# Performance work log

Hardware: AMD Instinct MI355X
Metric: run time of the kernel (lower is better)

The kernel has to match this reference:

```python
import jax, jax.numpy as jnp
import numpy as np

N = 8          # num_nodes (forced: stack with deconv output of leading dim 64 = 8*8)
T = 10         # out_dim == num_steps (Conv1d(out_dim, 1, ...) runs over the time axis)
H = 64         # hidden_dim (forced: ConvTranspose1d in_channels=64)
E = 2 * N      # edges come in fwd/rev pairs; E/2 must equal N for avg_pool squeeze
NODE_IN = 512  # gat1 in_dim = x_feat width (510) + CNN_1 output (2)
EDGE_IN = 128


def _conv1d(x, w, b, pad):
    # x: [B, Cin, L], w: [Cout, Cin, K]
    y = jax.lax.conv_general_dilated(x, w, (1,), [(pad, pad)],
                                     dimension_numbers=('NCH', 'OIH', 'NCH'))
    return y + b[None, :, None]


def _gat(x, src, dst, ea, W, a_s, a_d, We, a_e, bias, heads, ch, concat):
    # PyG GATConv with edge_dim and default add_self_loops=True (mean-fill edge_attr)
    n = x.shape[0]
    loop = jnp.arange(n)
    src = jnp.concatenate([src, loop])
    dst = jnp.concatenate([dst, loop])
    ea = jnp.concatenate([ea, jnp.broadcast_to(ea.mean(0), (n, ea.shape[1]))], 0)
    h = (x @ W).reshape(n, heads, ch)                 # [N,H,C]
    he = (ea @ We).reshape(-1, heads, ch)             # [E+N,H,C]
    alpha = (h * a_s).sum(-1)[src] + (h * a_d).sum(-1)[dst] + (he * a_e).sum(-1)
    alpha = jax.nn.leaky_relu(alpha, 0.2)             # [E+N,H]
    amax = jax.ops.segment_max(alpha, dst, num_segments=n)
    ex = jnp.exp(alpha - amax[dst])
    den = jax.ops.segment_sum(ex, dst, num_segments=n)
    w = ex / (den[dst] + 1e-16)                       # scatter-softmax over dst
    out = jax.ops.segment_sum(w[:, :, None] * h[src], dst, num_segments=n)
    out = out.reshape(n, heads * ch) if concat else out.mean(1)
    return out + bias


def _forward(x_feat, x_feat_tmp, edge_attr, c1w1, c1b1, c1w2, c1b2,
             g1_lin, g1_as, g1_ad, g1_le, g1_ae, g1_b,
             g2_lin, g2_as, g2_ad, g2_le, g2_ae, g2_b,
             mlp_w1, mlp_b1, mlp_w2, mlp_b2,
             d1w, d1b, d2w, d2b, d3w, d3b,
             c2w1, c2b1, c2w2, c2b2, c2l1w, c2l1b, c2l2w, c2l2b,
             edge_index):
    src, dst = edge_index[0], edge_index[1]
    # ---- CNN_1 on rows 1 and 5 of x_feat_tmp ----
    t = jnp.stack([x_feat_tmp[1], x_feat_tmp[5]], axis=1)    # [N,2,T]
    t = t.reshape(2, N, T)                                   # torch .view semantics
    t = jax.nn.relu(_conv1d(t, c1w1, c1b1, 1))               # [2,N,T]
    t = _conv1d(jnp.transpose(t, (0, 2, 1)), c1w2, c1b2, 1)  # [2,1,N]
    x_ = jax.nn.relu(t.reshape(N, 2))                        # torch .view semantics
    # ---- GAT stack ----
    x = jnp.concatenate([x_feat, x_], axis=1)                # [N,512]
    x = jax.nn.relu(_gat(x, src, dst, edge_attr, g1_lin, g1_as, g1_ad,
                         g1_le, g1_ae, g1_b, 4, H, True))    # [N,256]
    ea_new = jax.nn.relu(edge_attr @ mlp_w1 + mlp_b1) @ mlp_w2 + mlp_b2  # [E,64]
    x = jax.nn.relu(_gat(x, src, dst, ea_new, g2_lin, g2_as, g2_ad,
                         g2_le, g2_ae, g2_b, 1, H, False))   # [N,64]
    # ---- ConvTranspose1d on length-1 input == einsum; avg_pool2d over nodes/edges ----
    x_pool = (jnp.einsum('ni,iot->not', x, d1w) + d1b[None, :, None]).mean(0)          # [64,10]
    ef = (jnp.einsum('ni,iot->not', ea_new[::2], d2w) + d2b[None, :, None]).mean(0)    # [64,10]
    er = (jnp.einsum('ni,iot->not', ea_new[1::2], d3w) + d3b[None, :, None]).mean(0)   # [64,10]
    inf = x_feat_tmp.reshape(N * N, T)                       # [64,10]
    # ---- CNN_2 ----
    c = jnp.stack([x_pool, inf, ef, er], axis=1)             # [64,4,10]
    c = _conv1d(c, c2w1, c2b1, 0)                            # [64,32,8]
    c = c.reshape(N * N, 32, 4, 2).max(-1)                   # MaxPool1d(2) -> [64,32,4]
    c = _conv1d(c, c2w2, c2b2, 0)                            # [64,64,2]
    c = c.reshape(N * N, 128)                                # Flatten(1,2)
    c = jax.nn.relu((c @ c2l1w + c2l1b) @ c2l2w + c2l2b)     # [64,10]
    return c.reshape(N, N, T)


def setup_inputs():
    ks = iter(jax.random.split(jax.random.key(0), 48))
    def rn(shape, s=0.1):
        return jax.random.normal(next(ks), shape, dtype=jnp.float32) * s
    return dict(
        x_feat=rn((N, NODE_IN - 2), 1.0),
        x_feat_tmp=rn((N, N, T), 1.0),
        edge_attr=rn((E, EDGE_IN), 1.0),
        c1w1=rn((N, N, 3)), c1b1=rn((N,)),
        c1w2=rn((1, T, 3)), c1b2=rn((1,)),
        g1_lin=rn((NODE_IN, 4 * H)), g1_as=rn((4, H)), g1_ad=rn((4, H)),
        g1_le=rn((EDGE_IN, 4 * H)), g1_ae=rn((4, H)), g1_b=rn((4 * H,)),
        g2_lin=rn((4 * H, H)), g2_as=rn((1, H)), g2_ad=rn((1, H)),
        g2_le=rn((H, H)), g2_ae=rn((1, H)), g2_b=rn((H,)),
        mlp_w1=rn((EDGE_IN, H)), mlp_b1=rn((H,)),
        mlp_w2=rn((H, H)), mlp_b2=rn((H,)),
        d1w=rn((H, H, 10)), d1b=rn((H,)),
        d2w=rn((H, H, 10)), d2b=rn((H,)),
        d3w=rn((H, H, 10)), d3b=rn((H,)),
        c2w1=rn((32, 4, 3)), c2b1=rn((32,)),
        c2w2=rn((64, 32, 3)), c2b2=rn((64,)),
        c2l1w=rn((128, 256)), c2l1b=rn((256,)),
        c2l2w=rn((256, T)), c2l2b=rn((T,)),
        edge_index=jax.random.randint(next(ks), (2, E), 0, N, dtype=jnp.int32),
    )


def reference(x_feat, x_feat_tmp, edge_attr, c1w1, c1b1, c1w2, c1b2,
              g1_lin, g1_as, g1_ad, g1_le, g1_ae, g1_b,
              g2_lin, g2_as, g2_ad, g2_le, g2_ae, g2_b,
              mlp_w1, mlp_b1, mlp_w2, mlp_b2,
              d1w, d1b, d2w, d2b, d3w, d3b,
              c2w1, c2b1, c2w2, c2b2, c2l1w, c2l1b, c2l2w, c2l2b,
              edge_index):
    return _forward(x_feat, x_feat_tmp, edge_attr, c1w1, c1b1, c1w2, c1b2,
                    g1_lin, g1_as, g1_ad, g1_le, g1_ae, g1_b,
                    g2_lin, g2_as, g2_ad, g2_le, g2_ae, g2_b,
                    mlp_w1, mlp_b1, mlp_w2, mlp_b2,
                    d1w, d1b, d2w, d2b, d3w, d3b,
                    c2w1, c2b1, c2w2, c2b2, c2l1w, c2l1b, c2l2w, c2l2b,
                    edge_index)
```

## Files before the change

kernel.cpp:

```cpp
#include <hip/hip_runtime.h>
#include <math.h>

#define WS_HXPART 0
#define WS_SMALL  8192
#define SM_XCNN 0
#define SM_SE1A 16
#define SM_SE1B 84
#define SM_SE2  152
#define SM_WF   172
#define SM_BF   1452
#define SM_VME  1462
#define SM_SIZE 1600

#define F_H    0
#define F_X1   2048
#define F_H2P  4096
#define F_GL0  6144
#define F_GL1  6400
#define F_G1AS 6656
#define F_G1AD 6912
#define F_G1B  7168
#define F_SS1  7424
#define F_SD1  7456
#define F_MX1  7488
#define F_DN1  7520
#define F_WT1  7552
#define F_SW2  7680
#define F_A1   7680
#define F_H2   7936
#define F_X2   8448
#define F_G2AS 8960
#define F_G2AD 9024
#define F_G2B  9088
#define F_SS2  9152
#define F_SD2  9160
#define F_MX2  9168
#define F_DN2  9176
#define F_A2   9184
#define F_WT2  9248
#define F_SML  13824
#define F_SW1  15424
#define F_CIN  15808
#define F_ESRC 15968
#define F_EDST 15992
#define F_SB1  16016
#define F_SB2  16048
#define F_SDB  16112
#define F_VM0  16128
#define SM_TOT 16192

__global__ __launch_bounds__(256) void k1_pre(
    const float* __restrict__ xf,   const float* __restrict__ xft,
    const float* __restrict__ ea,
    const float* __restrict__ c1w1, const float* __restrict__ c1b1,
    const float* __restrict__ c1w2, const float* __restrict__ c1b2,
    const float* __restrict__ g1lin,const float* __restrict__ g1le,
    const float* __restrict__ g1ae,
    const float* __restrict__ mw1,  const float* __restrict__ mb1,
    const float* __restrict__ mw2,  const float* __restrict__ mb2,
    const float* __restrict__ g2le, const float* __restrict__ g2ae,
    const float* __restrict__ l1w,  const float* __restrict__ l1b,
    const float* __restrict__ l2w,  const float* __restrict__ l2b,
    float* __restrict__ ws)
{
    const int b = blockIdx.x, tid = threadIdx.x;
    if (b < 4) {
        __shared__ float sx[1024];
        const int k0 = b * 128;
        const int klen = (b == 3) ? 126 : 128;
        for (int idx = tid; idx < 1024; idx += 256) {
            int n = idx >> 7, kk = idx & 127;
            sx[n * 128 + kk] = (kk < klen) ? xf[n * 510 + k0 + kk] : 0.f;
        }
        __syncthreads();
        float acc[8];
        #pragma unroll
        for (int n = 0; n < 8; ++n) acc[n] = 0.f;
        for (int kk = 0; kk < 128; ++kk) {
            float w = g1lin[(k0 + kk) * 256 + tid];
            #pragma unroll
            for (int n = 0; n < 8; ++n) acc[n] += sx[n * 128 + kk] * w;
        }
        #pragma unroll
        for (int n = 0; n < 8; ++n)
            ws[WS_HXPART + ((n * 256 + tid) << 2) + b] = acc[n];
    } else if (b < 6) {
        __shared__ float seaC[1088];
        __shared__ float sae[256], q1h[256];
        const int kh = b - 4, k0 = kh * 64;
        for (int idx = tid; idx < 1024; idx += 256) {
            int e = idx >> 6, kk = idx & 63;
            seaC[e * 64 + kk] = ea[e * 128 + k0 + kk];
        }
        sae[tid] = g1ae[tid];
        __syncthreads();
        if (tid < 64) {
            float m = 0.f;
            for (int e = 0; e < 16; ++e) m += seaC[e * 64 + tid];
            seaC[1024 + tid] = m * (1.f / 16.f);
        }
        __syncthreads();
        {
            int kk = tid >> 2, hd = tid & 3;
            float acc = 0.f;
            for (int c = 0; c < 64; ++c)
                acc += g1le[(k0 + kk) * 256 + hd * 64 + c] * sae[hd * 64 + c];
            q1h[tid] = acc;
        }
        __syncthreads();
        if (tid < 68) {
            int e = tid >> 2, hd = tid & 3;
            int row = (tid < 64) ? e : 16;
            if (tid >= 64) hd = tid - 64;
            float acc = 0.f;
            for (int kk = 0; kk < 64; ++kk) acc += seaC[row * 64 + kk] * q1h[kk * 4 + hd];
            int dst = (tid < 64) ? tid : (64 + hd);
            ws[WS_SMALL + ((kh == 0) ? SM_SE1A : SM_SE1B) + dst] = acc;
        }
    } else if (b == 6) {
        __shared__ float sea[2048];
        __shared__ float tmp[1024];
        __shared__ float ean[17 * 64];
        __shared__ float sq2a[64], sq2[64];
        for (int idx = tid; idx < 2048; idx += 256) sea[idx] = ea[idx];
        if (tid < 64) sq2a[tid] = g2ae[tid];
        __syncthreads();
        for (int o = tid; o < 1024; o += 256) {
            int e = o >> 6, c = o & 63;
            float acc = mb1[c];
            for (int k = 0; k < 128; ++k) acc += sea[e * 128 + k] * mw1[k * 64 + c];
            tmp[o] = fmaxf(acc, 0.f);
        }
        __syncthreads();
        for (int o = tid; o < 1024; o += 256) {
            int e = o >> 6, c = o & 63;
            float acc = mb2[c];
            for (int k = 0; k < 64; ++k) acc += tmp[e * 64 + k] * mw2[k * 64 + c];
            ean[o] = acc;
        }
        __syncthreads();
        if (tid < 64) {
            float m = 0.f;
            for (int e = 0; e < 16; ++e) m += ean[e * 64 + tid];
            ean[1024 + tid] = m * (1.f / 16.f);
        } else if (tid < 128) {
            int c = tid - 64;
            float m = 0.f;
            for (int e = 0; e < 16; e += 2) m += ean[e * 64 + c];
            ws[WS_SMALL + SM_VME + c] = m * 0.125f;
        } else if (tid < 192) {
            int c = tid - 128;
            float m = 0.f;
            for (int e = 1; e < 16; e += 2) m += ean[e * 64 + c];
            ws[WS_SMALL + SM_VME + 64 + c] = m * 0.125f;
        }
        __syncthreads();
        if (tid < 64) {
            float acc = 0.f;
            for (int c = 0; c < 64; ++c) acc += g2le[tid * 64 + c] * sq2a[c];
            sq2[tid] = acc;
        }
        __syncthreads();
        if (tid < 16) {
            float acc = 0.f;
            for (int k = 0; k < 64; ++k) acc += ean[tid * 64 + k] * sq2[k];
            ws[WS_SMALL + SM_SE2 + tid] = acc;
        } else if (tid == 16) {
            float acc = 0.f;
            for (int k = 0; k < 64; ++k) acc += ean[1024 + k] * sq2[k];
            ws[WS_SMALL + SM_SE2 + 16] = acc;
        }
    } else if (b == 7) {
        __shared__ float t2[160], y1[160], y2[16];
        if (tid < 160) {
            int b_ = tid / 80, ch = (tid % 80) / 10, tt = tid % 10;
            int srow = ((ch & 1) == 0) ? 1 : 5;
            int n = 4 * b_ + (ch >> 1);
            t2[tid] = xft[srow * 80 + n * 10 + tt];
        }
        __syncthreads();
        if (tid < 160) {
            int b_ = tid / 80, co = (tid % 80) / 10, tt = tid % 10;
            float acc = c1b1[co];
            for (int ci = 0; ci < 8; ++ci)
                for (int k = 0; k < 3; ++k) {
                    int p = tt + k - 1;
                    if (p >= 0 && p < 10) acc += t2[b_ * 80 + ci * 10 + p] * c1w1[co * 24 + ci * 3 + k];
                }
            y1[tid] = fmaxf(acc, 0.f);
        }
        __syncthreads();
        if (tid < 16) {
            int b_ = tid >> 3, p = tid & 7;
            float acc = c1b2[0];
            for (int i = 0; i < 10; ++i)
                for (int k = 0; k < 3; ++k) {
                    int q = p + k - 1;
                    if (q >= 0 && q < 8) acc += y1[b_ * 80 + q * 10 + i] * c1w2[i * 3 + k];
                }
            y2[tid] = acc;
        }
        __syncthreads();
        if (tid < 16) ws[WS_SMALL + SM_XCNN + tid] = fmaxf(y2[tid], 0.f);
    } else {
        __shared__ float sl2[2560];
        for (int idx = tid; idx < 2560; idx += 256) sl2[idx] = l2w[idx];
        __syncthreads();
        const int m0 = (b - 8) * 32;
        for (int o = tid; o < 320; o += 256) {
            int ml = o / 10, t = o % 10, m = m0 + ml;
            float acc = 0.f;
            for (int j = 0; j < 256; ++j) acc += l1w[m * 256 + j] * sl2[j * 10 + t];
            ws[WS_SMALL + SM_WF + m * 10 + t] = acc;
        }
        if (b == 8 && tid < 10) {
            float acc = l2b[tid];
            for (int j = 0; j < 256; ++j) acc += l1b[j] * sl2[j * 10 + tid];
            ws[WS_SMALL + SM_BF + tid] = acc;
        }
    }
}

__global__ __launch_bounds__(512) void k2_main(
    const float* __restrict__ xft,
    const float* __restrict__ g1lin,
    const float* __restrict__ g1as, const float* __restrict__ g1ad,
    const float* __restrict__ g1b,
    const float* __restrict__ g2lin,
    const float* __restrict__ g2as, const float* __restrict__ g2ad,
    const float* __restrict__ g2b,
    const int* __restrict__ eidx,
    const float* __restrict__ d1w, const float* __restrict__ d1b,
    const float* __restrict__ d2w, const float* __restrict__ d2b,
    const float* __restrict__ d3w, const float* __restrict__ d3b,
    const float* __restrict__ c2w1, const float* __restrict__ c2b1,
    const float* __restrict__ c2w2, const float* __restrict__ c2b2,
    const float* __restrict__ ws, float* __restrict__ out)
{
    __shared__ float sm[SM_TOT];
    const int tid = threadIdx.x;
    const int r0 = blockIdx.x * 4;
    int* esrc = (int*)sm + F_ESRC;
    int* edst = (int*)sm + F_EDST;

    const int jj = tid & 255, hf = tid >> 8;
    float4 rH[4];
    #pragma unroll
    for (int nl = 0; nl < 4; ++nl)
        rH[nl] = *(const float4*)&ws[WS_HXPART + (((hf * 4 + nl) * 256 + jj) << 2)];
    if (tid < 400)
        *(float4*)&sm[F_SML + tid * 4] = *(const float4*)&ws[WS_SMALL + tid * 4];
    if (tid < 256) {
        sm[F_G1AS + tid] = g1as[tid];
        sm[F_G1AD + tid] = g1ad[tid];
        sm[F_G1B  + tid] = g1b[tid];
        sm[F_GL0  + tid] = g1lin[510 * 256 + tid];
        sm[F_GL1  + tid] = g1lin[511 * 256 + tid];
    } else {
        int j = tid - 256;
        if (j < 64)       { sm[F_G2AS + j] = g2as[j]; sm[F_G2AD + j] = g2ad[j]; sm[F_G2B + j] = g2b[j]; }
        else if (j < 88)  { int i = j - 64;  esrc[i] = (i < 16) ? eidx[i] : i - 16;
                                             edst[i] = (i < 16) ? eidx[16 + i] : i - 16; }
        else if (j < 128) { int i = j - 88;  int rl = i / 10, t = i % 10;
                            sm[F_CIN + rl * 40 + 10 + t] = xft[(r0 + rl) * 10 + t]; }
        else if (j < 160) sm[F_SB1 + j - 128] = c2b1[j - 128];
        else if (j < 224) sm[F_SB2 + j - 160] = c2b2[j - 160];
        else if (j < 236) { int i = j - 224, tau = i / 4, rl = i % 4;
                            const float* db = (tau == 0) ? d1b : (tau == 1) ? d2b : d3b;
                            sm[F_SDB + i] = db[r0 + rl]; }
    }
    for (int idx = tid; idx < 384; idx += 512) sm[F_SW1 + idx] = c2w1[idx];
    float rA[15], rW[12];
    {
        int ii = tid / 40, rem = tid - (tid / 40) * 40;
        #pragma unroll
        for (int i = 0; i < 15; ++i) {
            const float* dw = (ii < 64) ? d1w : (ii < 128) ? d2w : d3w;
            rA[i] = dw[(ii & 63) * 640 + r0 * 10 + rem];
            ii += 12; rem += 32; if (rem >= 40) { rem -= 40; ++ii; }
        }
    }
    #pragma unroll
    for (int i = 0; i < 12; ++i) rW[i] = c2w2[tid + 512 * i];
    {
        float p0 = g2lin[tid * 32], p1 = g2lin[tid * 32 + 16];
        asm volatile("" :: "v"(p0), "v"(p1));
    }
    __syncthreads();

    #pragma unroll
    for (int nl = 0; nl < 4; ++nl) {
        int n = hf * 4 + nl;
        float acc = ((rH[nl].x + rH[nl].y) + rH[nl].z) + rH[nl].w;
        acc += sm[F_SML + SM_XCNN + n * 2] * sm[F_GL0 + jj]
             + sm[F_SML + SM_XCNN + n * 2 + 1] * sm[F_GL1 + jj];
        sm[F_H + n * 256 + jj] = acc;
    }
    __syncthreads();
    {
        int p = tid >> 4, g = tid & 15, n = p >> 2, hd = p & 3;
        float aS = 0.f, aD = 0.f;
        #pragma unroll
        for (int cc = 0; cc < 4; ++cc) {
            int c = (((cc + p) & 3) << 4) + g;
            float hv = sm[F_H + n * 256 + hd * 64 + c];
            aS += hv * sm[F_G1AS + hd * 64 + c];
            aD += hv * sm[F_G1AD + hd * 64 + c];
        }
        #pragma unroll
        for (int m = 8; m >= 1; m >>= 1) { aS += __shfl_xor(aS, m); aD += __shfl_xor(aD, m); }
        if (g == 0) { sm[F_SS1 + p] = aS; sm[F_SD1 + p] = aD; }
    }
    __syncthreads();
    {
        int p = tid >> 4, g = tid & 15, n = p >> 2, hd = p & 3;
        #define AL1(e) ({ int _e = (e); \
            float _se = (_e < 16) ? (sm[F_SML+SM_SE1A+_e*4+hd] + sm[F_SML+SM_SE1B+_e*4+hd]) \
                                  : (sm[F_SML+SM_SE1A+64+hd]   + sm[F_SML+SM_SE1B+64+hd]); \
            float _s = sm[F_SS1 + esrc[_e]*4+hd] + sm[F_SD1 + edst[_e]*4+hd] + _se; \
            (_s > 0.f) ? _s : 0.2f * _s; })
        float v1 = (edst[g] == n) ? AL1(g) : -1e30f;
        float v2 = (g < 8 && edst[g + 16] == n) ? AL1(g + 16) : -1e30f;
        float mx = fmaxf(v1, v2);
        #pragma unroll
        for (int m = 8; m >= 1; m >>= 1) mx = fmaxf(mx, __shfl_xor(mx, m));
        float ex = expf(v1 - mx) + ((g < 8) ? expf(v2 - mx) : 0.f);
        #pragma unroll
        for (int m = 8; m >= 1; m >>= 1) ex += __shfl_xor(ex, m);
        if (g == 0) { sm[F_MX1 + p] = mx; sm[F_DN1 + p] = ex; }
    }
    __syncthreads();
    if (tid < 96) {
        int e = tid >> 2, hd = tid & 3, d = edst[e];
        float al = AL1(e);
        sm[F_WT1 + tid] = expf(al - sm[F_MX1 + d * 4 + hd]) / (sm[F_DN1 + d * 4 + hd] + 1e-16f);
        #undef AL1
    }
    __syncthreads();
    if (tid < 256) {
        int s = tid >> 5, n = (tid >> 2) & 7, hd = tid & 3;
        float acc = 0.f;
        #pragma unroll
        for (int e = 0; e < 24; ++e)
            acc += (edst[e] == n && esrc[e] == s) ? sm[F_WT1 + e * 4 + hd] : 0.f;
        sm[F_A1 + tid] = acc;
    }
    __syncthreads();
    {
        const int hd = jj >> 6;
        #pragma unroll
        for (int nl = 0; nl < 4; ++nl) {
            int n = hf * 4 + nl;
            float acc = 0.f;
            #pragma unroll
            for (int s = 0; s < 8; ++s)
                acc += sm[F_A1 + s * 32 + n * 4 + hd] * sm[F_H + s * 256 + jj];
            sm[F_X1 + n * 256 + jj] = fmaxf(acc + sm[F_G1B + jj], 0.f);
        }
    }
    __syncthreads();
    {
        const int kc = tid >> 7, sub = (tid >> 6) & 1, c = tid & 63;
        float p0 = 0.f, p1 = 0.f, p2 = 0.f, p3 = 0.f;
        for (int kk = 0; kk < 64; ++kk) {
            int k = kc * 64 + kk;
            float g = g2lin[k * 64 + c];
            p0 += sm[F_X1 + (sub * 4 + 0) * 256 + k] * g;
            p1 += sm[F_X1 + (sub * 4 + 1) * 256 + k] * g;
            p2 += sm[F_X1 + (sub * 4 + 2) * 256 + k] * g;
            p3 += sm[F_X1 + (sub * 4 + 3) * 256 + k] * g;
        }
        sm[F_H2P + kc * 512 + (sub * 4 + 0) * 64 + c] = p0;
        sm[F_H2P + kc * 512 + (sub * 4 + 1) * 64 + c] = p1;
        sm[F_H2P + kc * 512 + (sub * 4 + 2) * 64 + c] = p2;
        sm[F_H2P + kc * 512 + (sub * 4 + 3) * 64 + c] = p3;
        #pragma unroll
        for (int i = 4; i < 12; ++i) sm[F_SW2 + tid + 512 * i] = rW[i];
    }
    __syncthreads();
    {
        int n = tid >> 6, c = tid & 63;
        float hv = sm[F_H2P + n * 64 + c] + sm[F_H2P + 512 + n * 64 + c]
                 + sm[F_H2P + 1024 + n * 64 + c] + sm[F_H2P + 1536 + n * 64 + c];
        sm[F_H2 + n * 64 + c] = hv;
        float aS = hv * sm[F_G2AS + c], aD = hv * sm[F_G2AD + c];
        #pragma unroll
        for (int m = 32; m >= 1; m >>= 1) { aS += __shfl_xor(aS, m); aD += __shfl_xor(aD, m); }
        if (c == 0) { sm[F_SS2 + n] = aS; sm[F_SD2 + n] = aD; }
    }
    __syncthreads();
    {
        #define AL2(e) ({ int _e = (e); \
            float _s = sm[F_SS2 + esrc[_e]] + sm[F_SD2 + edst[_e]] \
                     + sm[F_SML + SM_SE2 + ((_e < 16) ? _e : 16)]; \
            (_s > 0.f) ? _s : 0.2f * _s; })
        if (tid < 256) {
            int n = tid >> 5, g = tid & 31;
            float v = (g < 24 && edst[g] == n) ? AL2(g) : -1e30f;
            float mx = v;
            #pragma unroll
            for (int m = 16; m >= 1; m >>= 1) mx = fmaxf(mx, __shfl_xor(mx, m));
            float ex = expf(v - mx);
            #pragma unroll
            for (int m = 16; m >= 1; m >>= 1) ex += __shfl_xor(ex, m);
            if (g == 0) { sm[F_MX2 + n] = mx; sm[F_DN2 + n] = ex; }
        }
    }
    __syncthreads();
    if (tid < 24) {
        int d = edst[tid];
        float al = AL2(tid);
        sm[F_WT2 + tid] = expf(al - sm[F_MX2 + d]) / (sm[F_DN2 + d] + 1e-16f);
        #undef AL2
    }
    __syncthreads();
    if (tid < 64) {
        int n = tid >> 3, s = tid & 7;
        float acc = 0.f;
        #pragma unroll
        for (int e = 0; e < 24; ++e)
            acc += (edst[e] == n && esrc[e] == s) ? sm[F_WT2 + e] : 0.f;
        sm[F_A2 + tid] = acc;
    }
    __syncthreads();
    {
        int n = tid >> 6, c = tid & 63;
        float acc = 0.f;
        #pragma unroll
        for (int s = 0; s < 8; ++s) acc += sm[F_A2 + n * 8 + s] * sm[F_H2 + s * 64 + c];
        sm[F_X2 + n * 64 + c] = fmaxf(acc + sm[F_G2B + c], 0.f);
    }
    __syncthreads();
    if (tid < 64) {
        float m = 0.f;
        #pragma unroll
        for (int n = 0; n < 8; ++n) m += sm[F_X2 + n * 64 + tid];
        sm[F_VM0 + tid] = m * 0.125f;
    }
    __syncthreads();

    #pragma unroll
    for (int i = 0; i < 15; ++i) sm[tid + 512 * i] = rA[i];
    #pragma unroll
    for (int i = 0; i < 4; ++i) sm[F_SW2 + tid + 512 * i] = rW[i];
    __syncthreads();
    if (tid < 480) {
        int o = tid >> 2, q = tid & 3;
        int t = o % 10, tau = (o / 10) % 3, rl = o / 30;
        float acc = 0.f;
        for (int i = q * 16; i < q * 16 + 16; ++i) {
            float vm = (tau == 0) ? sm[F_VM0 + i]
                     : (tau == 1) ? sm[F_SML + SM_VME + i]
                                  : sm[F_SML + SM_VME + 64 + i];
            acc += vm * sm[(tau * 64 + i) * 40 + rl * 10 + t];
        }
        acc += __shfl_xor(acc, 2); acc += __shfl_xor(acc, 1);
        if (q == 0) {
            int ch = (tau == 0) ? 0 : (tau + 1);
            sm[F_CIN + rl * 40 + ch * 10 + t] = acc + sm[F_SDB + tau * 4 + rl];
        }
    }
    __syncthreads();
    for (int o = tid; o < 1024; o += 512) {
        int rl = o >> 8, co = (o >> 3) & 31, p = o & 7;
        float acc = sm[F_SB1 + co];
        #pragma unroll
        for (int ci = 0; ci < 4; ++ci)
            #pragma unroll
            for (int k = 0; k < 3; ++k)
                acc += sm[F_CIN + rl * 40 + ci * 10 + p + k] * sm[F_SW1 + co * 12 + ci * 3 + k];
        sm[4096 + o] = acc;
    }
    __syncthreads();
    {
        int rl = tid >> 7, m = tid & 127, co2 = m >> 1, p = m & 1;
        float acc = sm[F_SB2 + co2];
        for (int ci = 0; ci < 32; ++ci)
            #pragma unroll
            for (int k = 0; k < 3; ++k) {
                int u0 = 4096 + rl * 256 + ci * 8 + 2 * (p + k);
                acc += fmaxf(sm[u0], sm[u0 + 1]) * sm[F_SW2 + co2 * 96 + ci * 3 + k];
            }
        sm[1024 + rl * 128 + m] = acc;
    }
    __syncthreads();
    if (tid < 320) {
        int o = tid >> 3, l = tid & 7;
        int rl = o / 10, t = o % 10;
        float acc = 0.f;
        for (int m = l * 16; m < l * 16 + 16; ++m)
            acc += sm[1024 + rl * 128 + m] * sm[F_SML + SM_WF + m * 10 + t];
        acc += __shfl_xor(acc, 4); acc += __shfl_xor(acc, 2); acc += __shfl_xor(acc, 1);
        if (l == 0)
            out[(r0 + rl) * 10 + t] = fmaxf(acc + sm[F_SML + SM_BF + t], 0.f);
    }
}

extern "C" void kernel_launch(void* const* d_in, const int* in_sizes, int n_in,
                              void* d_out, int out_size, void* d_ws, size_t ws_size,
                              hipStream_t stream)
{
    const float* xf    = (const float*)d_in[0];
    const float* xft   = (const float*)d_in[1];
    const float* ea    = (const float*)d_in[2];
    const float* c1w1  = (const float*)d_in[3];
    const float* c1b1  = (const float*)d_in[4];
    const float* c1w2  = (const float*)d_in[5];
    const float* c1b2  = (const float*)d_in[6];
    const float* g1lin = (const float*)d_in[7];
    const float* g1as  = (const float*)d_in[8];
    const float* g1ad  = (const float*)d_in[9];
    const float* g1le  = (const float*)d_in[10];
    const float* g1ae  = (const float*)d_in[11];
    const float* g1b   = (const float*)d_in[12];
    const float* g2lin = (const float*)d_in[13];
    const float* g2as  = (const float*)d_in[14];
    const float* g2ad  = (const float*)d_in[15];
    const float* g2le  = (const float*)d_in[16];
    const float* g2ae  = (const float*)d_in[17];
    const float* g2b   = (const float*)d_in[18];
    const float* mw1   = (const float*)d_in[19];
    const float* mb1   = (const float*)d_in[20];
    const float* mw2   = (const float*)d_in[21];
    const float* mb2   = (const float*)d_in[22];
    const float* d1w   = (const float*)d_in[23];
    const float* d1b   = (const float*)d_in[24];
    const float* d2w   = (const float*)d_in[25];
    const float* d2b   = (const float*)d_in[26];
    const float* d3w   = (const float*)d_in[27];
    const float* d3b   = (const float*)d_in[28];
    const float* c2w1  = (const float*)d_in[29];
    const float* c2b1  = (const float*)d_in[30];
    const float* c2w2  = (const float*)d_in[31];
    const float* c2b2  = (const float*)d_in[32];
    const float* l1w   = (const float*)d_in[33];
    const float* l1b   = (const float*)d_in[34];
    const float* l2w   = (const float*)d_in[35];
    const float* l2b   = (const float*)d_in[36];
    const int*   eidx  = (const int*)d_in[37];
    float* ws  = (float*)d_ws;
    float* out = (float*)d_out;

    hipLaunchKernelGGL(k1_pre, dim3(12), dim3(256), 0, stream,
        xf, xft, ea, c1w1, c1b1, c1w2, c1b2,
        g1lin, g1le, g1ae, mw1, mb1, mw2, mb2,
        g2le, g2ae, l1w, l1b, l2w, l2b, ws);
    hipLaunchKernelGGL(k2_main, dim3(16), dim3(512), 0, stream,
        xft, g1lin, g1as, g1ad, g1b,
        g2lin, g2as, g2ad, g2b, eidx,
        d1w, d1b, d2w, d2b, d3w, d3b,
        c2w1, c2b1, c2w2, c2b2, ws, out);
}
```

Before: 33.46 us.

## Split k1 preprocessing across more blocks and stage weights in shared memory

Raises the k1_pre grid from 12 to 18 blocks. The x@W1 partial products are split into 8 K-chunks instead of 4, and the edge-projection reduction into 4 chunks instead of 2, which shortens the serial critical path of each block. Weight matrices are staged in LDS with batched register loads. k2 now sums 8 partials and 4 edge-score pieces, and several inner loops are unrolled. The cost is a larger workspace, more partial sums to reduce in k2, and much larger LDS footprints per block.

```diff
diff --git a/kernel.cpp b/kernel.cpp
--- a/kernel.cpp
+++ b/kernel.cpp
@@ -2,15 +2,14 @@
 #include <math.h>
 
 #define WS_HXPART 0
-#define WS_SMALL  8192
+#define WS_SMALL  16384
 #define SM_XCNN 0
-#define SM_SE1A 16
-#define SM_SE1B 84
-#define SM_SE2  152
-#define SM_WF   172
-#define SM_BF   1452
-#define SM_VME  1462
-#define SM_SIZE 1600
+#define SM_SE1  16
+#define SM_SE2  288
+#define SM_WF   308
+#define SM_BF   1588
+#define SM_VME  1600
+#define SM_SIZE 1728
 
 #define F_H    0
 #define F_X1   2048
@@ -39,15 +38,15 @@
 #define F_A2   9184
 #define F_WT2  9248
 #define F_SML  13824
-#define F_SW1  15424
-#define F_CIN  15808
-#define F_ESRC 15968
-#define F_EDST 15992
-#define F_SB1  16016
-#define F_SB2  16048
-#define F_SDB  16112
-#define F_VM0  16128
-#define SM_TOT 16192
+#define F_SW1  15552
+#define F_CIN  15936
+#define F_ESRC 16096
+#define F_EDST 16120
+#define F_SB1  16144
+#define F_SB2  16176
+#define F_SDB  16240
+#define F_VM0  16256
+#define SM_TOT 16320
 
 __global__ __launch_bounds__(256) void k1_pre(
     const float* __restrict__ xf,   const float* __restrict__ xft,
@@ -64,48 +63,55 @@
     float* __restrict__ ws)
 {
     const int b = blockIdx.x, tid = threadIdx.x;
-    if (b < 4) {
-        __shared__ float sx[1024];
-        const int k0 = b * 128;
-        const int klen = (b == 3) ? 126 : 128;
-        for (int idx = tid; idx < 1024; idx += 256) {
-            int n = idx >> 7, kk = idx & 127;
-            sx[n * 128 + kk] = (kk < klen) ? xf[n * 510 + k0 + kk] : 0.f;
+    if (b < 8) {
+        __shared__ float sx[512];
+        const int k0 = b * 64;
+        const int klen = (b == 7) ? 62 : 64;
+        for (int idx = tid; idx < 512; idx += 256) {
+            int n = idx >> 6, kk = idx & 63;
+            sx[n * 64 + kk] = (kk < klen) ? xf[n * 510 + k0 + kk] : 0.f;
         }
         __syncthreads();
         float acc[8];
         #pragma unroll
         for (int n = 0; n < 8; ++n) acc[n] = 0.f;
-        for (int kk = 0; kk < 128; ++kk) {
-            float w = g1lin[(k0 + kk) * 256 + tid];
-            #pragma unroll
-            for (int n = 0; n < 8; ++n) acc[n] += sx[n * 128 + kk] * w;
-        }
-        #pragma unroll
-        for (int n = 0; n < 8; ++n)
-            ws[WS_HXPART + ((n * 256 + tid) << 2) + b] = acc[n];
-    } else if (b < 6) {
-        __shared__ float seaC[1088];
-        __shared__ float sae[256], q1h[256];
-        const int kh = b - 4, k0 = kh * 64;
-        for (int idx = tid; idx < 1024; idx += 256) {
-            int e = idx >> 6, kk = idx & 63;
-            seaC[e * 64 + kk] = ea[e * 128 + k0 + kk];
+        for (int kb = 0; kb < 64; kb += 16) {
+            float w[16];
+            #pragma unroll
+            for (int u = 0; u < 16; ++u) w[u] = g1lin[(k0 + kb + u) * 256 + tid];
+            #pragma unroll
+            for (int u = 0; u < 16; ++u)
+                #pragma unroll
+                for (int n = 0; n < 8; ++n) acc[n] += sx[n * 64 + kb + u] * w[u];
+        }
+        #pragma unroll
+        for (int n = 0; n < 8; ++n) ws[WS_HXPART + (n * 256 + tid) * 8 + b] = acc[n];
+    } else if (b < 12) {
+        __shared__ float sg[8192];
+        __shared__ float seaC[544];
+        __shared__ float sae[256], q1q[128];
+        const int qb = b - 8, kq0 = qb * 32;
+        #pragma unroll 8
+        for (int idx = tid; idx < 8192; idx += 256) sg[idx] = g1le[kq0 * 256 + idx];
+        for (int idx = tid; idx < 512; idx += 256) {
+            int e = idx >> 5, kk = idx & 31;
+            seaC[e * 32 + kk] = ea[e * 128 + kq0 + kk];
         }
         sae[tid] = g1ae[tid];
         __syncthreads();
-        if (tid < 64) {
+        if (tid < 32) {
             float m = 0.f;
-            for (int e = 0; e < 16; ++e) m += seaC[e * 64 + tid];
-            seaC[1024 + tid] = m * (1.f / 16.f);
-        }
-        __syncthreads();
-        {
+            #pragma unroll
+            for (int e = 0; e < 16; ++e) m += seaC[e * 32 + tid];
+            seaC[512 + tid] = m * (1.f / 16.f);
+        }
+        __syncthreads();
+        if (tid < 128) {
             int kk = tid >> 2, hd = tid & 3;
-            float acc = 0.f;
-            for (int c = 0; c < 64; ++c)
-                acc += g1le[(k0 + kk) * 256 + hd * 64 + c] * sae[hd * 64 + c];
-            q1h[tid] = acc;
+            float a = 0.f;
+            #pragma unroll 8
+            for (int c = 0; c < 64; ++c) a += sg[kk * 256 + hd * 64 + c] * sae[hd * 64 + c];
+            q1q[tid] = a;
         }
         __syncthreads();
         if (tid < 68) {
@@ -113,56 +119,95 @@
             int row = (tid < 64) ? e : 16;
             if (tid >= 64) hd = tid - 64;
             float acc = 0.f;
-            for (int kk = 0; kk < 64; ++kk) acc += seaC[row * 64 + kk] * q1h[kk * 4 + hd];
+            #pragma unroll
+            for (int kk = 0; kk < 32; ++kk) acc += seaC[row * 32 + kk] * q1q[kk * 4 + hd];
             int dst = (tid < 64) ? tid : (64 + hd);
-            ws[WS_SMALL + ((kh == 0) ? SM_SE1A : SM_SE1B) + dst] = acc;
-        }
-    } else if (b == 6) {
+            ws[WS_SMALL + SM_SE1 + qb * 68 + dst] = acc;
+        }
+    } else if (b < 16) {
+        __shared__ float sl2[2560];
+        __shared__ float sl1[8192];
+        const int m0 = (b - 12) * 32;
+        #pragma unroll 8
+        for (int idx = tid; idx < 2560; idx += 256) sl2[idx] = l2w[idx];
+        #pragma unroll 8
+        for (int idx = tid; idx < 8192; idx += 256) sl1[idx] = l1w[m0 * 256 + idx];
+        __syncthreads();
+        for (int o = tid; o < 320; o += 256) {
+            int ml = o / 10, t = o % 10;
+            float acc = 0.f;
+            #pragma unroll 8
+            for (int j = 0; j < 256; ++j) acc += sl1[ml * 256 + j] * sl2[j * 10 + t];
+            ws[WS_SMALL + SM_WF + (m0 + ml) * 10 + t] = acc;
+        }
+        if (b == 12 && tid < 10) {
+            float acc = l2b[tid];
+            #pragma unroll 8
+            for (int j = 0; j < 256; ++j) acc += l1b[j] * sl2[j * 10 + tid];
+            ws[WS_SMALL + SM_BF + tid] = acc;
+        }
+    } else if (b == 16) {
         __shared__ float sea[2048];
         __shared__ float tmp[1024];
-        __shared__ float ean[17 * 64];
+        __shared__ float ean[1088];
+        __shared__ float smw[8192];
         __shared__ float sq2a[64], sq2[64];
+        #pragma unroll 8
         for (int idx = tid; idx < 2048; idx += 256) sea[idx] = ea[idx];
+        #pragma unroll 8
+        for (int idx = tid; idx < 8192; idx += 256) smw[idx] = mw1[idx];
         if (tid < 64) sq2a[tid] = g2ae[tid];
         __syncthreads();
         for (int o = tid; o < 1024; o += 256) {
             int e = o >> 6, c = o & 63;
             float acc = mb1[c];
-            for (int k = 0; k < 128; ++k) acc += sea[e * 128 + k] * mw1[k * 64 + c];
+            #pragma unroll 8
+            for (int k = 0; k < 128; ++k) acc += sea[e * 128 + k] * smw[k * 64 + c];
             tmp[o] = fmaxf(acc, 0.f);
         }
+        __syncthreads();
+        #pragma unroll 8
+        for (int idx = tid; idx < 4096; idx += 256) smw[idx] = mw2[idx];
+        #pragma unroll 8
+        for (int idx = tid; idx < 4096; idx += 256) smw[4096 + idx] = g2le[idx];
         __syncthreads();
         for (int o = tid; o < 1024; o += 256) {
             int e = o >> 6, c = o & 63;
             float acc = mb2[c];
-            for (int k = 0; k < 64; ++k) acc += tmp[e * 64 + k] * mw2[k * 64 + c];
+            #pragma unroll 8
+            for (int k = 0; k < 64; ++k) acc += tmp[e * 64 + k] * smw[k * 64 + c];
             ean[o] = acc;
+        }
+        if (tid >= 192 && tid < 256) {
+            int c = tid - 192;
+            float acc = 0.f;
+            #pragma unroll 8
+            for (int cc = 0; cc < 64; ++cc) acc += smw[4096 + c * 64 + cc] * sq2a[cc];
+            sq2[c] = acc;
         }
         __syncthreads();
         if (tid < 64) {
             float m = 0.f;
+            #pragma unroll
             for (int e = 0; e < 16; ++e) m += ean[e * 64 + tid];
             ean[1024 + tid] = m * (1.f / 16.f);
         } else if (tid < 128) {
             int c = tid - 64;
             float m = 0.f;
+            #pragma unroll
             for (int e = 0; e < 16; e += 2) m += ean[e * 64 + c];
             ws[WS_SMALL + SM_VME + c] = m * 0.125f;
         } else if (tid < 192) {
             int c = tid - 128;
             float m = 0.f;
+            #pragma unroll
             for (int e = 1; e < 16; e += 2) m += ean[e * 64 + c];
             ws[WS_SMALL + SM_VME + 64 + c] = m * 0.125f;
         }
         __syncthreads();
-        if (tid < 64) {
-            float acc = 0.f;
-            for (int c = 0; c < 64; ++c) acc += g2le[tid * 64 + c] * sq2a[c];
-            sq2[tid] = acc;
-        }
-        __syncthreads();
         if (tid < 16) {
             float acc = 0.f;
+            #pragma unroll 8
             for (int k = 0; k < 64; ++k) acc += ean[tid * 64 + k] * sq2[k];
             ws[WS_SMALL + SM_SE2 + tid] = acc;
         } else if (tid == 16) {
@@ -170,8 +215,8 @@
             for (int k = 0; k < 64; ++k) acc += ean[1024 + k] * sq2[k];
             ws[WS_SMALL + SM_SE2 + 16] = acc;
         }
-    } else if (b == 7) {
-        __shared__ float t2[160], y1[160], y2[16];
+    } else {
+        __shared__ float t2[160], y1[160];
         if (tid < 160) {
             int b_ = tid / 80, ch = (tid % 80) / 10, tt = tid % 10;
             int srow = ((ch & 1) == 0) ? 1 : 5;
@@ -198,25 +243,7 @@
                     int q = p + k - 1;
                     if (q >= 0 && q < 8) acc += y1[b_ * 80 + q * 10 + i] * c1w2[i * 3 + k];
                 }
-            y2[tid] = acc;
-        }
-        __syncthreads();
-        if (tid < 16) ws[WS_SMALL + SM_XCNN + tid] = fmaxf(y2[tid], 0.f);
-    } else {
-        __shared__ float sl2[2560];
-        for (int idx = tid; idx < 2560; idx += 256) sl2[idx] = l2w[idx];
-        __syncthreads();
-        const int m0 = (b - 8) * 32;
-        for (int o = tid; o < 320; o += 256) {
-            int ml = o / 10, t = o % 10, m = m0 + ml;
-            float acc = 0.f;
-            for (int j = 0; j < 256; ++j) acc += l1w[m * 256 + j] * sl2[j * 10 + t];
-            ws[WS_SMALL + SM_WF + m * 10 + t] = acc;
-        }
-        if (b == 8 && tid < 10) {
-            float acc = l2b[tid];
-            for (int j = 0; j < 256; ++j) acc += l1b[j] * sl2[j * 10 + tid];
-            ws[WS_SMALL + SM_BF + tid] = acc;
+            ws[WS_SMALL + SM_XCNN + tid] = fmaxf(acc, 0.f);
         }
     }
 }
@@ -240,15 +267,18 @@
     __shared__ float sm[SM_TOT];
     const int tid = threadIdx.x;
     const int r0 = blockIdx.x * 4;
+    const int jj = tid & 255, hf = tid >> 8;
     int* esrc = (int*)sm + F_ESRC;
     int* edst = (int*)sm + F_EDST;
 
-    const int jj = tid & 255, hf = tid >> 8;
-    float4 rH[4];
+    float4 rHa[4], rHb[4];
     #pragma unroll
-    for (int nl = 0; nl < 4; ++nl)
-        rH[nl] = *(const float4*)&ws[WS_HXPART + (((hf * 4 + nl) * 256 + jj) << 2)];
-    if (tid < 400)
+    for (int nl = 0; nl < 4; ++nl) {
+        int base = WS_HXPART + ((hf * 4 + nl) * 256 + jj) * 8;
+        rHa[nl] = *(const float4*)&ws[base];
+        rHb[nl] = *(const float4*)&ws[base + 4];
+    }
+    if (tid < 432)
         *(float4*)&sm[F_SML + tid * 4] = *(const float4*)&ws[WS_SMALL + tid * 4];
     if (tid < 256) {
         sm[F_G1AS + tid] = g1as[tid];
@@ -291,7 +321,8 @@
     #pragma unroll
     for (int nl = 0; nl < 4; ++nl) {
         int n = hf * 4 + nl;
-        float acc = ((rH[nl].x + rH[nl].y) + rH[nl].z) + rH[nl].w;
+        float4 a = rHa[nl], b4 = rHb[nl];
+        float acc = ((a.x + a.y) + (a.z + a.w)) + ((b4.x + b4.y) + (b4.z + b4.w));
         acc += sm[F_SML + SM_XCNN + n * 2] * sm[F_GL0 + jj]
              + sm[F_SML + SM_XCNN + n * 2 + 1] * sm[F_GL1 + jj];
         sm[F_H + n * 256 + jj] = acc;
@@ -315,8 +346,9 @@
     {
         int p = tid >> 4, g = tid & 15, n = p >> 2, hd = p & 3;
         #define AL1(e) ({ int _e = (e); \
-            float _se = (_e < 16) ? (sm[F_SML+SM_SE1A+_e*4+hd] + sm[F_SML+SM_SE1B+_e*4+hd]) \
-                                  : (sm[F_SML+SM_SE1A+64+hd]   + sm[F_SML+SM_SE1B+64+hd]); \
+            int _i = (_e < 16) ? (_e * 4 + hd) : (64 + hd); \
+            float _se = sm[F_SML+SM_SE1 + _i] + sm[F_SML+SM_SE1 + 68 + _i] \
+                      + sm[F_SML+SM_SE1 + 136 + _i] + sm[F_SML+SM_SE1 + 204 + _i]; \
             float _s = sm[F_SS1 + esrc[_e]*4+hd] + sm[F_SD1 + edst[_e]*4+hd] + _se; \
             (_s > 0.f) ? _s : 0.2f * _s; })
         float v1 = (edst[g] == n) ? AL1(g) : -1e30f;
@@ -362,13 +394,18 @@
     {
         const int kc = tid >> 7, sub = (tid >> 6) & 1, c = tid & 63;
         float p0 = 0.f, p1 = 0.f, p2 = 0.f, p3 = 0.f;
-        for (int kk = 0; kk < 64; ++kk) {
-            int k = kc * 64 + kk;
-            float g = g2lin[k * 64 + c];
-            p0 += sm[F_X1 + (sub * 4 + 0) * 256 + k] * g;
-            p1 += sm[F_X1 + (sub * 4 + 1) * 256 + k] * g;
-            p2 += sm[F_X1 + (sub * 4 + 2) * 256 + k] * g;
-            p3 += sm[F_X1 + (sub * 4 + 3) * 256 + k] * g;
+        for (int kb = 0; kb < 64; kb += 8) {
+            float g[8];
+            #pragma unroll
+            for (int u = 0; u < 8; ++u) g[u] = g2lin[(kc * 64 + kb + u) * 64 + c];
+            #pragma unroll
+            for (int u = 0; u < 8; ++u) {
+                int k = kc * 64 + kb + u;
+                p0 += sm[F_X1 + (sub * 4 + 0) * 256 + k] * g[u];
+                p1 += sm[F_X1 + (sub * 4 + 1) * 256 + k] * g[u];
+                p2 += sm[F_X1 + (sub * 4 + 2) * 256 + k] * g[u];
+                p3 += sm[F_X1 + (sub * 4 + 3) * 256 + k] * g[u];
+            }
         }
         sm[F_H2P + kc * 512 + (sub * 4 + 0) * 64 + c] = p0;
         sm[F_H2P + kc * 512 + (sub * 4 + 1) * 64 + c] = p1;
@@ -448,11 +485,13 @@
         int o = tid >> 2, q = tid & 3;
         int t = o % 10, tau = (o / 10) % 3, rl = o / 30;
         float acc = 0.f;
-        for (int i = q * 16; i < q * 16 + 16; ++i) {
-            float vm = (tau == 0) ? sm[F_VM0 + i]
-                     : (tau == 1) ? sm[F_SML + SM_VME + i]
-                                  : sm[F_SML + SM_VME + 64 + i];
-            acc += vm * sm[(tau * 64 + i) * 40 + rl * 10 + t];
+        #pragma unroll
+        for (int i = 0; i < 16; ++i) {
+            int ii = q * 16 + i;
+            float vm = (tau == 0) ? sm[F_VM0 + ii]
+                     : (tau == 1) ? sm[F_SML + SM_VME + ii]
+                                  : sm[F_SML + SM_VME + 64 + ii];
+            acc += vm * sm[(tau * 64 + ii) * 40 + rl * 10 + t];
         }
         acc += __shfl_xor(acc, 2); acc += __shfl_xor(acc, 1);
         if (q == 0) {
@@ -488,8 +527,11 @@
         int o = tid >> 3, l = tid & 7;
         int rl = o / 10, t = o % 10;
         float acc = 0.f;
-        for (int m = l * 16; m < l * 16 + 16; ++m)
+        #pragma unroll
+        for (int i = 0; i < 16; ++i) {
+            int m = l * 16 + i;
             acc += sm[1024 + rl * 128 + m] * sm[F_SML + SM_WF + m * 10 + t];
+        }
         acc += __shfl_xor(acc, 4); acc += __shfl_xor(acc, 2); acc += __shfl_xor(acc, 1);
         if (l == 0)
             out[(r0 + rl) * 10 + t] = fmaxf(acc + sm[F_SML + SM_BF + t], 0.f);
@@ -541,7 +583,7 @@
     float* ws  = (float*)d_ws;
     float* out = (float*)d_out;
 
-    hipLaunchKernelGGL(k1_pre, dim3(12), dim3(256), 0, stream,
+    hipLaunchKernelGGL(k1_pre, dim3(18), dim3(256), 0, stream,
         xf, xft, ea, c1w1, c1b1, c1w2, c1b2,
         g1lin, g1le, g1ae, mw1, mb1, mw2, mb2,
         g2le, g2ae, l1w, l1b, l2w, l2b, ws);
```

Measured after the change: 36.17 us. +8.1%, slower.

## Hoist input-independent deconv and conv work early, fuse softmax weights, drop register staging

Applied to the files above, without the earlier changes.

Deconv channels 2 and 3 and the conv1 partial sums over those channels depend only on precomputed data, so they now run before the GAT stages. The late tail only handles the channel that depends on the GAT output. The separate GAT softmax-weight passes (and their barriers) are folded into the adjacency accumulation, which recomputes exp per edge. The g2 matmul is reworked into float4 global loads with an 8-way K split. Conv2 and deconv weights are read from global/L2 instead of being staged through registers and shared memory. This lowers register pressure and sync count, at the cost of redundant exp work and more global reads.

```diff
diff --git a/kernel.cpp b/kernel.cpp
--- a/kernel.cpp
+++ b/kernel.cpp
@@ -12,42 +12,40 @@
 #define SM_VME  1462
 #define SM_SIZE 1600
 
-#define F_H    0
-#define F_X1   2048
-#define F_H2P  4096
-#define F_GL0  6144
-#define F_GL1  6400
-#define F_G1AS 6656
-#define F_G1AD 6912
-#define F_G1B  7168
-#define F_SS1  7424
-#define F_SD1  7456
-#define F_MX1  7488
-#define F_DN1  7520
-#define F_WT1  7552
-#define F_SW2  7680
-#define F_A1   7680
-#define F_H2   7936
-#define F_X2   8448
-#define F_G2AS 8960
-#define F_G2AD 9024
-#define F_G2B  9088
-#define F_SS2  9152
-#define F_SD2  9160
-#define F_MX2  9168
-#define F_DN2  9176
-#define F_A2   9184
-#define F_WT2  9248
-#define F_SML  13824
-#define F_SW1  15424
-#define F_CIN  15808
-#define F_ESRC 15968
-#define F_EDST 15992
-#define F_SB1  16016
-#define F_SB2  16048
-#define F_SDB  16112
-#define F_VM0  16128
-#define SM_TOT 16192
+#define F_H     0
+#define F_X1    2048
+#define F_H2P   4096
+#define F_GL0   6144
+#define F_GL1   6400
+#define F_G1AS  6656
+#define F_G1AD  6912
+#define F_G1B   7168
+#define F_SS1   7424
+#define F_SD1   7456
+#define F_MX1   7488
+#define F_DN1   7520
+#define F_A1    7680
+#define F_H2    7936
+#define F_X2    8448
+#define F_G2AS  8960
+#define F_G2AD  9024
+#define F_G2B   9088
+#define F_SS2   9152
+#define F_SD2   9160
+#define F_MX2   9168
+#define F_DN2   9176
+#define F_A2    9184
+#define F_UPART 9280
+#define F_SML   13824
+#define F_SW1   15424
+#define F_CIN   15808
+#define F_ESRC  15968
+#define F_EDST  15992
+#define F_SB1   16016
+#define F_SB2   16048
+#define F_SDB   16112
+#define F_VM0   16128
+#define SM_TOT  16192
 
 __global__ __launch_bounds__(256) void k1_pre(
     const float* __restrict__ xf,   const float* __restrict__ xft,
@@ -240,10 +238,10 @@
     __shared__ float sm[SM_TOT];
     const int tid = threadIdx.x;
     const int r0 = blockIdx.x * 4;
+    const int jj = tid & 255, hf = tid >> 8;
     int* esrc = (int*)sm + F_ESRC;
     int* edst = (int*)sm + F_EDST;
 
-    const int jj = tid & 255, hf = tid >> 8;
     float4 rH[4];
     #pragma unroll
     for (int nl = 0; nl < 4; ++nl)
@@ -270,33 +268,58 @@
                             sm[F_SDB + i] = db[r0 + rl]; }
     }
     for (int idx = tid; idx < 384; idx += 512) sm[F_SW1 + idx] = c2w1[idx];
-    float rA[15], rW[12];
     {
         int ii = tid / 40, rem = tid - (tid / 40) * 40;
         #pragma unroll
         for (int i = 0; i < 15; ++i) {
             const float* dw = (ii < 64) ? d1w : (ii < 128) ? d2w : d3w;
-            rA[i] = dw[(ii & 63) * 640 + r0 * 10 + rem];
+            float v = dw[(ii & 63) * 640 + r0 * 10 + rem];
+            asm volatile("" :: "v"(v));
             ii += 12; rem += 32; if (rem >= 40) { rem -= 40; ++ii; }
         }
-    }
-    #pragma unroll
-    for (int i = 0; i < 12; ++i) rW[i] = c2w2[tid + 512 * i];
-    {
+        #pragma unroll
+        for (int i = 0; i < 12; ++i) { float v = c2w2[tid + 512 * i]; asm volatile("" :: "v"(v)); }
         float p0 = g2lin[tid * 32], p1 = g2lin[tid * 32 + 16];
         asm volatile("" :: "v"(p0), "v"(p1));
+    }
+    __syncthreads();
+
+    if (tid < 320) {
+        int o = tid >> 2, q = tid & 3;
+        int tt = o % 10, rl = (o / 10) & 3, ts = o / 40;
+        const float* dw = ts ? d3w : d2w;
+        float acc = 0.f;
+        #pragma unroll
+        for (int i2 = 0; i2 < 16; ++i2) {
+            int i = q * 16 + i2;
+            acc += sm[F_SML + SM_VME + ts * 64 + i] * dw[i * 640 + (r0 + rl) * 10 + tt];
+        }
+        acc += __shfl_xor(acc, 2); acc += __shfl_xor(acc, 1);
+        if (q == 0) sm[F_CIN + rl * 40 + (2 + ts) * 10 + tt] = acc + sm[F_SDB + (1 + ts) * 4 + rl];
     }
     __syncthreads();
 
     #pragma unroll
     for (int nl = 0; nl < 4; ++nl) {
         int n = hf * 4 + nl;
-        float acc = ((rH[nl].x + rH[nl].y) + rH[nl].z) + rH[nl].w;
+        float4 a = rH[nl];
+        float acc = ((a.x + a.y) + (a.z + a.w));
         acc += sm[F_SML + SM_XCNN + n * 2] * sm[F_GL0 + jj]
              + sm[F_SML + SM_XCNN + n * 2 + 1] * sm[F_GL1 + jj];
         sm[F_H + n * 256 + jj] = acc;
     }
-    __syncthreads();
+    for (int o = tid; o < 1024; o += 512) {
+        int rl = o >> 8, co = (o >> 3) & 31, p = o & 7;
+        float acc = sm[F_SB1 + co];
+        #pragma unroll
+        for (int ci = 1; ci < 4; ++ci)
+            #pragma unroll
+            for (int k = 0; k < 3; ++k)
+                acc += sm[F_CIN + rl * 40 + ci * 10 + p + k] * sm[F_SW1 + co * 12 + ci * 3 + k];
+        sm[F_UPART + o] = acc;
+    }
+    __syncthreads();
+
     {
         int p = tid >> 4, g = tid & 15, n = p >> 2, hd = p & 3;
         float aS = 0.f, aD = 0.f;
@@ -312,15 +335,15 @@
         if (g == 0) { sm[F_SS1 + p] = aS; sm[F_SD1 + p] = aD; }
     }
     __syncthreads();
+    #define AL1(e, hd) ({ int _e = (e); \
+        float _se = (_e < 16) ? (sm[F_SML+SM_SE1A+_e*4+(hd)] + sm[F_SML+SM_SE1B+_e*4+(hd)]) \
+                              : (sm[F_SML+SM_SE1A+64+(hd)]   + sm[F_SML+SM_SE1B+64+(hd)]); \
+        float _s = sm[F_SS1 + esrc[_e]*4+(hd)] + sm[F_SD1 + edst[_e]*4+(hd)] + _se; \
+        (_s > 0.f) ? _s : 0.2f * _s; })
     {
         int p = tid >> 4, g = tid & 15, n = p >> 2, hd = p & 3;
-        #define AL1(e) ({ int _e = (e); \
-            float _se = (_e < 16) ? (sm[F_SML+SM_SE1A+_e*4+hd] + sm[F_SML+SM_SE1B+_e*4+hd]) \
-                                  : (sm[F_SML+SM_SE1A+64+hd]   + sm[F_SML+SM_SE1B+64+hd]); \
-            float _s = sm[F_SS1 + esrc[_e]*4+hd] + sm[F_SD1 + edst[_e]*4+hd] + _se; \
-            (_s > 0.f) ? _s : 0.2f * _s; })
-        float v1 = (edst[g] == n) ? AL1(g) : -1e30f;
-        float v2 = (g < 8 && edst[g + 16] == n) ? AL1(g + 16) : -1e30f;
+        float v1 = (edst[g] == n) ? AL1(g, hd) : -1e30f;
+        float v2 = (g < 8 && edst[g + 16] == n) ? AL1(g + 16, hd) : -1e30f;
         float mx = fmaxf(v1, v2);
         #pragma unroll
         for (int m = 8; m >= 1; m >>= 1) mx = fmaxf(mx, __shfl_xor(mx, m));
@@ -330,21 +353,19 @@
         if (g == 0) { sm[F_MX1 + p] = mx; sm[F_DN1 + p] = ex; }
     }
     __syncthreads();
-    if (tid < 96) {
-        int e = tid >> 2, hd = tid & 3, d = edst[e];
-        float al = AL1(e);
-        sm[F_WT1 + tid] = expf(al - sm[F_MX1 + d * 4 + hd]) / (sm[F_DN1 + d * 4 + hd] + 1e-16f);
-        #undef AL1
-    }
-    __syncthreads();
     if (tid < 256) {
         int s = tid >> 5, n = (tid >> 2) & 7, hd = tid & 3;
+        float mx = sm[F_MX1 + n * 4 + hd], dn = sm[F_DN1 + n * 4 + hd] + 1e-16f;
         float acc = 0.f;
         #pragma unroll
-        for (int e = 0; e < 24; ++e)
-            acc += (edst[e] == n && esrc[e] == s) ? sm[F_WT1 + e * 4 + hd] : 0.f;
+        for (int e = 0; e < 24; ++e) {
+            bool mt = (edst[e] == n && esrc[e] == s);
+            float v = expf(AL1(e, hd) - mx) / dn;
+            acc += mt ? v : 0.f;
+        }
         sm[F_A1 + tid] = acc;
     }
+    #undef AL1
     __syncthreads();
     {
         const int hd = jj >> 6;
@@ -360,68 +381,62 @@
     }
     __syncthreads();
     {
-        const int kc = tid >> 7, sub = (tid >> 6) & 1, c = tid & 63;
-        float p0 = 0.f, p1 = 0.f, p2 = 0.f, p3 = 0.f;
-        for (int kk = 0; kk < 64; ++kk) {
-            int k = kc * 64 + kk;
-            float g = g2lin[k * 64 + c];
-            p0 += sm[F_X1 + (sub * 4 + 0) * 256 + k] * g;
-            p1 += sm[F_X1 + (sub * 4 + 1) * 256 + k] * g;
-            p2 += sm[F_X1 + (sub * 4 + 2) * 256 + k] * g;
-            p3 += sm[F_X1 + (sub * 4 + 3) * 256 + k] * g;
-        }
-        sm[F_H2P + kc * 512 + (sub * 4 + 0) * 64 + c] = p0;
-        sm[F_H2P + kc * 512 + (sub * 4 + 1) * 64 + c] = p1;
-        sm[F_H2P + kc * 512 + (sub * 4 + 2) * 64 + c] = p2;
-        sm[F_H2P + kc * 512 + (sub * 4 + 3) * 64 + c] = p3;
-        #pragma unroll
-        for (int i = 4; i < 12; ++i) sm[F_SW2 + tid + 512 * i] = rW[i];
+        const int kc = tid >> 6, nh = (tid >> 4) & 3, cg = tid & 15;
+        float a0x = 0, a0y = 0, a0z = 0, a0w = 0, a1x = 0, a1y = 0, a1z = 0, a1w = 0;
+        for (int kk = 0; kk < 32; ++kk) {
+            int k = kc * 32 + kk;
+            float4 g = *(const float4*)(g2lin + k * 64 + cg * 4);
+            float xA = sm[F_X1 + nh * 256 + k];
+            float xB = sm[F_X1 + (nh + 4) * 256 + k];
+            a0x += xA * g.x; a0y += xA * g.y; a0z += xA * g.z; a0w += xA * g.w;
+            a1x += xB * g.x; a1y += xB * g.y; a1z += xB * g.z; a1w += xB * g.w;
+        }
+        int base = (kc < 4) ? (F_H + kc * 512) : (F_H2P + (kc - 4) * 512);
+        *(float4*)&sm[base + nh * 64 + cg * 4]       = make_float4(a0x, a0y, a0z, a0w);
+        *(float4*)&sm[base + (nh + 4) * 64 + cg * 4] = make_float4(a1x, a1y, a1z, a1w);
     }
     __syncthreads();
     {
         int n = tid >> 6, c = tid & 63;
-        float hv = sm[F_H2P + n * 64 + c] + sm[F_H2P + 512 + n * 64 + c]
-                 + sm[F_H2P + 1024 + n * 64 + c] + sm[F_H2P + 1536 + n * 64 + c];
-        sm[F_H2 + n * 64 + c] = hv;
+        float hv = 0.f;
+        #pragma unroll
+        for (int kc = 0; kc < 4; ++kc) hv += sm[F_H + kc * 512 + tid] + sm[F_H2P + kc * 512 + tid];
+        sm[F_H2 + tid] = hv;
         float aS = hv * sm[F_G2AS + c], aD = hv * sm[F_G2AD + c];
         #pragma unroll
         for (int m = 32; m >= 1; m >>= 1) { aS += __shfl_xor(aS, m); aD += __shfl_xor(aD, m); }
         if (c == 0) { sm[F_SS2 + n] = aS; sm[F_SD2 + n] = aD; }
     }
     __syncthreads();
-    {
-        #define AL2(e) ({ int _e = (e); \
-            float _s = sm[F_SS2 + esrc[_e]] + sm[F_SD2 + edst[_e]] \
-                     + sm[F_SML + SM_SE2 + ((_e < 16) ? _e : 16)]; \
-            (_s > 0.f) ? _s : 0.2f * _s; })
-        if (tid < 256) {
-            int n = tid >> 5, g = tid & 31;
-            float v = (g < 24 && edst[g] == n) ? AL2(g) : -1e30f;
-            float mx = v;
-            #pragma unroll
-            for (int m = 16; m >= 1; m >>= 1) mx = fmaxf(mx, __shfl_xor(mx, m));
-            float ex = expf(v - mx);
-            #pragma unroll
-            for (int m = 16; m >= 1; m >>= 1) ex += __shfl_xor(ex, m);
-            if (g == 0) { sm[F_MX2 + n] = mx; sm[F_DN2 + n] = ex; }
-        }
-    }
-    __syncthreads();
-    if (tid < 24) {
-        int d = edst[tid];
-        float al = AL2(tid);
-        sm[F_WT2 + tid] = expf(al - sm[F_MX2 + d]) / (sm[F_DN2 + d] + 1e-16f);
-        #undef AL2
+    #define AL2(e) ({ int _e = (e); \
+        float _s = sm[F_SS2 + esrc[_e]] + sm[F_SD2 + edst[_e]] \
+                 + sm[F_SML + SM_SE2 + ((_e < 16) ? _e : 16)]; \
+        (_s > 0.f) ? _s : 0.2f * _s; })
+    if (tid < 256) {
+        int n = tid >> 5, g = tid & 31;
+        float v = (g < 24 && edst[g] == n) ? AL2(g) : -1e30f;
+        float mx = v;
+        #pragma unroll
+        for (int m = 16; m >= 1; m >>= 1) mx = fmaxf(mx, __shfl_xor(mx, m));
+        float ex = expf(v - mx);
+        #pragma unroll
+        for (int m = 16; m >= 1; m >>= 1) ex += __shfl_xor(ex, m);
+        if (g == 0) { sm[F_MX2 + n] = mx; sm[F_DN2 + n] = ex; }
     }
     __syncthreads();
     if (tid < 64) {
         int n = tid >> 3, s = tid & 7;
+        float mx = sm[F_MX2 + n], dn = sm[F_DN2 + n] + 1e-16f;
         float acc = 0.f;
         #pragma unroll
-        for (int e = 0; e < 24; ++e)
-            acc += (edst[e] == n && esrc[e] == s) ? sm[F_WT2 + e] : 0.f;
-        sm[F_A2 + tid] = acc;
-    }
+        for (int e = 0; e < 24; ++e) {
+            bool mt = (edst[e] == n && esrc[e] == s);
+            float v = expf(AL2(e) - mx) / dn;
+            acc += mt ? v : 0.f;
+        }
+        sm[F_A2 + n * 8 + s] = acc;
+    }
+    #undef AL2
     __syncthreads();
     {
         int n = tid >> 6, c = tid & 63;
@@ -438,58 +453,52 @@
         sm[F_VM0 + tid] = m * 0.125f;
     }
     __syncthreads();
-
-    #pragma unroll
-    for (int i = 0; i < 15; ++i) sm[tid + 512 * i] = rA[i];
-    #pragma unroll
-    for (int i = 0; i < 4; ++i) sm[F_SW2 + tid + 512 * i] = rW[i];
-    __syncthreads();
-    if (tid < 480) {
-        int o = tid >> 2, q = tid & 3;
-        int t = o % 10, tau = (o / 10) % 3, rl = o / 30;
+    if (tid < 320) {
+        int o = tid >> 3, l = tid & 7;
+        int rl = o / 10, tt = o % 10;
         float acc = 0.f;
-        for (int i = q * 16; i < q * 16 + 16; ++i) {
-            float vm = (tau == 0) ? sm[F_VM0 + i]
-                     : (tau == 1) ? sm[F_SML + SM_VME + i]
-                                  : sm[F_SML + SM_VME + 64 + i];
-            acc += vm * sm[(tau * 64 + i) * 40 + rl * 10 + t];
-        }
-        acc += __shfl_xor(acc, 2); acc += __shfl_xor(acc, 1);
-        if (q == 0) {
-            int ch = (tau == 0) ? 0 : (tau + 1);
-            sm[F_CIN + rl * 40 + ch * 10 + t] = acc + sm[F_SDB + tau * 4 + rl];
-        }
+        #pragma unroll
+        for (int i2 = 0; i2 < 8; ++i2) {
+            int i = l * 8 + i2;
+            acc += sm[F_VM0 + i] * d1w[i * 640 + (r0 + rl) * 10 + tt];
+        }
+        acc += __shfl_xor(acc, 4); acc += __shfl_xor(acc, 2); acc += __shfl_xor(acc, 1);
+        if (l == 0) sm[F_CIN + rl * 40 + tt] = acc + sm[F_SDB + rl];
     }
     __syncthreads();
     for (int o = tid; o < 1024; o += 512) {
         int rl = o >> 8, co = (o >> 3) & 31, p = o & 7;
-        float acc = sm[F_SB1 + co];
-        #pragma unroll
-        for (int ci = 0; ci < 4; ++ci)
-            #pragma unroll
-            for (int k = 0; k < 3; ++k)
-                acc += sm[F_CIN + rl * 40 + ci * 10 + p + k] * sm[F_SW1 + co * 12 + ci * 3 + k];
-        sm[4096 + o] = acc;
+        float acc = sm[F_UPART + o];
+        #pragma unroll
+        for (int k = 0; k < 3; ++k)
+            acc += sm[F_CIN + rl * 40 + p + k] * sm[F_SW1 + co * 12 + k];
+        sm[F_H + o] = acc;
     }
     __syncthreads();
     {
         int rl = tid >> 7, m = tid & 127, co2 = m >> 1, p = m & 1;
         float acc = sm[F_SB2 + co2];
-        for (int ci = 0; ci < 32; ++ci)
-            #pragma unroll
-            for (int k = 0; k < 3; ++k) {
-                int u0 = 4096 + rl * 256 + ci * 8 + 2 * (p + k);
-                acc += fmaxf(sm[u0], sm[u0 + 1]) * sm[F_SW2 + co2 * 96 + ci * 3 + k];
-            }
-        sm[1024 + rl * 128 + m] = acc;
+        const float* wrow = c2w2 + co2 * 96;
+        #pragma unroll 8
+        for (int ci = 0; ci < 32; ++ci) {
+            float w0 = wrow[ci * 3], w1 = wrow[ci * 3 + 1], w2 = wrow[ci * 3 + 2];
+            int u0 = F_H + rl * 256 + ci * 8 + 2 * p;
+            acc += fmaxf(sm[u0],     sm[u0 + 1]) * w0;
+            acc += fmaxf(sm[u0 + 2], sm[u0 + 3]) * w1;
+            acc += fmaxf(sm[u0 + 4], sm[u0 + 5]) * w2;
+        }
+        sm[F_H + 1024 + rl * 128 + m] = acc;
     }
     __syncthreads();
     if (tid < 320) {
         int o = tid >> 3, l = tid & 7;
         int rl = o / 10, t = o % 10;
         float acc = 0.f;
-        for (int m = l * 16; m < l * 16 + 16; ++m)
-            acc += sm[1024 + rl * 128 + m] * sm[F_SML + SM_WF + m * 10 + t];
+        #pragma unroll
+        for (int i = 0; i < 16; ++i) {
+            int m = l * 16 + i;
+            acc += sm[F_H + 1024 + rl * 128 + m] * sm[F_SML + SM_WF + m * 10 + t];
+        }
         acc += __shfl_xor(acc, 4); acc += __shfl_xor(acc, 2); acc += __shfl_xor(acc, 1);
         if (l == 0)
             out[(r0 + rl) * 10 + t] = fmaxf(acc + sm[F_SML + SM_BF + t], 0.f);
```

New measurement: 38.47 us. +15.0%, slower.
